# Optimization experiments

Hardware: AMD Instinct MI355X
Metric: run time of the kernel (lower is better)

Reference implementation:

```python
import jax, jax.numpy as jnp
import numpy as np

D = 128       # embed_dim
UD = 128      # user_embed_dim
NU, NI, NR = 100000, 50000, 10
B, H, S = 4096, 50, 32
EPS = 1e-5


def setup_inputs() -> dict:
    key = jax.random.key(0)
    ks = jax.random.split(key, 24)
    p = lambda k, s: (jax.random.normal(k, s, jnp.float32) * 0.05)
    inp = {
        'u2e': p(ks[0], (NU, D)), 'v2e': p(ks[1], (NI, D)), 'r2e': p(ks[2], (NR, D)),
        'gv_w1': p(ks[3], (2 * D, D)), 'gv_b1': jnp.zeros(D),
        'gv_w2': p(ks[4], (D, D)), 'gv_b2': jnp.zeros(D),
        'atth_w1': p(ks[5], (2 * D, D)), 'atth_b1': jnp.zeros(D),
        'atth_w2': p(ks[6], (D, 1)), 'atth_b2': jnp.zeros(1),
        'enc_w': p(ks[7], (2 * D, D)), 'enc_b': jnp.zeros(D),
        'atts_w1': p(ks[8], (2 * D, D)), 'atts_b1': jnp.zeros(D),
        'atts_w2': p(ks[9], (D, 1)), 'atts_b2': jnp.zeros(1),
        'soc_w': p(ks[10], (2 * D, D)), 'soc_b': jnp.zeros(D),
        'attn_wa': p(ks[11], (D, D)), 'attn_ba': p(ks[12], (D,)),
        'fc1_w': p(ks[13], (D, D)), 'fc1_b': jnp.zeros(D),
        'bn1_g': jnp.ones(D), 'bn1_b': jnp.zeros(D),
        'fc2_w': p(ks[14], (D, UD)), 'fc2_b': jnp.zeros(UD),
        'efc1_w': p(ks[15], (2 * UD, D)), 'efc1_b': jnp.zeros(D),
        'bn2_g': jnp.ones(D), 'bn2_b': jnp.zeros(D),
        'efc2_w': p(ks[16], (D, UD)), 'efc2_b': jnp.zeros(UD),
        'user_ids': jax.random.randint(ks[17], (B, 2), 0, NU),
        'hist_items': jax.random.randint(ks[18], (2 * B, H), 0, NI),
        'hist_ratings': jax.random.randint(ks[19], (2 * B, H), 0, NR),
        'soc_neigh': jax.random.randint(ks[20], (2 * B, S), 0, NU),
    }
    return inp


def _forward(u2e, v2e, r2e, gv_w1, gv_b1, gv_w2, gv_b2, atth_w1, atth_b1, atth_w2, atth_b2,
             enc_w, enc_b, atts_w1, atts_b1, atts_w2, atts_b2, soc_w, soc_b, attn_wa, attn_ba,
             fc1_w, fc1_b, bn1_g, bn1_b, fc2_w, fc2_b, efc1_w, efc1_b, bn2_g, bn2_b,
             efc2_w, efc2_b, user_ids, hist_items, hist_ratings, soc_neigh):
    u = u2e[user_ids.reshape(-1)]                                   # [N,D]
    # --- UV_Aggregator: rating-history aggregation with attention ---
    x = jnp.concatenate([v2e[hist_items], r2e[hist_ratings]], -1)   # [N,H,2D]
    x = jax.nn.relu(x @ gv_w1 + gv_b1)
    x = jax.nn.relu(x @ gv_w2 + gv_b2)                              # [N,H,D]
    q = jnp.broadcast_to(u[:, None, :], x.shape)
    e = jax.nn.relu(jnp.concatenate([x, q], -1) @ atth_w1 + atth_b1) @ atth_w2 + atth_b2
    a = jax.nn.softmax(e, axis=1)                                   # [N,H,1]
    agg = jnp.sum(a * x, axis=1)                                    # [N,D]
    # --- UV_Encoder ---
    h_hist = jax.nn.relu(jnp.concatenate([u, agg], -1) @ enc_w + enc_b)
    # --- Social_Aggregator: neighbor aggregation with attention ---
    nf = u2e[soc_neigh]                                             # [N,S,D]
    qn = jnp.broadcast_to(u[:, None, :], nf.shape)
    es = jax.nn.relu(jnp.concatenate([nf, qn], -1) @ atts_w1 + atts_b1) @ atts_w2 + atts_b2
    a_s = jax.nn.softmax(es, axis=1)
    agg_s = jnp.sum(a_s * nf, axis=1)                               # [N,D]
    # --- Social_Encoder ---
    h = jax.nn.relu(jnp.concatenate([h_hist, agg_s], -1) @ soc_w + soc_b)
    hp = h.reshape(-1, 2, D)                                        # [B,2,D] (initiator, respondent)
    # --- SelfAttentionBatch over each pair ---
    ap = jax.nn.softmax(jnp.tanh(hp @ attn_wa) @ attn_ba, axis=1)   # [B,2]
    w = ap[..., None] * hp                                          # [B,2,D]
    # --- social project head: fc1 -> BN (per-pair batch of 2, train mode) -> relu -> fc2 ---
    y = w @ fc1_w + fc1_b                                           # [B,2,D]
    mu = y.mean(axis=1, keepdims=True)
    var = y.var(axis=1, keepdims=True)
    y = (y - mu) * jax.lax.rsqrt(var + EPS) * bn1_g + bn1_b
    y = jax.nn.relu(y) @ fc2_w + fc2_b                              # [B,2,UD]
    ini, res = y[:, 0], y[:, 1]
    # --- esocial head on concatenated pair reps: fc -> BN over batch -> relu -> fc ---
    c = y.reshape(y.shape[0], -1)                                   # [B,2*UD]
    z = c @ efc1_w + efc1_b                                         # [B,D]
    z = (z - z.mean(0)) * jax.lax.rsqrt(z.var(0) + EPS) * bn2_g + bn2_b
    z = jax.nn.relu(z) @ efc2_w + efc2_b                            # [B,UD]
    return z, ini, res


def reference(u2e, v2e, r2e, gv_w1, gv_b1, gv_w2, gv_b2, atth_w1, atth_b1, atth_w2, atth_b2,
              enc_w, enc_b, atts_w1, atts_b1, atts_w2, atts_b2, soc_w, soc_b, attn_wa, attn_ba,
              fc1_w, fc1_b, bn1_g, bn1_b, fc2_w, fc2_b, efc1_w, efc1_b, bn2_g, bn2_b,
              efc2_w, efc2_b, user_ids, hist_items, hist_ratings, soc_neigh):
    return _forward(u2e, v2e, r2e, gv_w1, gv_b1, gv_w2, gv_b2, atth_w1, atth_b1, atth_w2,
                    atth_b2, enc_w, enc_b, atts_w1, atts_b1, atts_w2, atts_b2, soc_w, soc_b,
                    attn_wa, attn_ba, fc1_w, fc1_b, bn1_g, bn1_b, fc2_w, fc2_b, efc1_w,
                    efc1_b, bn2_g, bn2_b, efc2_w, efc2_b, user_ids, hist_items,
                    hist_ratings, soc_neigh)
```

## Files before the change

### kernel.cpp

```cpp
#include <hip/hip_runtime.h>
#include <hip/hip_bf16.h>
#include <math.h>

#define NROWS   8192
#define HLEN    50
#define SLEN    32
#define NPAIR   4096

typedef __attribute__((ext_vector_type(8))) short   short8;
typedef __attribute__((ext_vector_type(8))) __bf16  b8;
typedef __attribute__((ext_vector_type(4))) float   f32x4;
typedef unsigned short us;

#define A_GV_B1    0
#define A_GV_B2    128
#define A_ATTH_B1  256
#define A_ATTH_W2  384
#define A_ENC_W    512
#define A_ENC_B    33280
#define A_ATTS_B1  33408
#define A_ATTS_W2  33536
#define A_SOC_W    33664
#define A_SOC_B    66432
#define A_ATTN_WA  66560
#define A_ATTN_BA  82944
#define A_FC1_W    83072
#define A_FC1_B    99456
#define A_BN1_G    99584
#define A_BN1_B    99712
#define A_FC2_W    99840
#define A_FC2_B    116224
#define A_EFC1_W   116352
#define A_EFC1_B   149120
#define A_BN2_G    149248
#define A_BN2_B    149376
#define A_EFC2_W   149504
#define A_EFC2_B   165888
#define A_TOTAL    166016

#define WS_HR    0u
#define WS_Z     2097152u
#define WS_ST    4194304u
#define WS_WP1   4195328u
#define WS_WP2   4260864u
#define WS_WPA   4293632u
#define WS_WPS   4359168u
#define WS_AR    4424704u
#define WS_UB    4757504u
#define WS_VB    30357504u
#define WS_RB    43157504u
#define WS2_NEED 43160064u

__device__ __forceinline__ float b2f(us u){
  unsigned int x = ((unsigned int)u) << 16; float f;
  __builtin_memcpy(&f, &x, 4); return f;
}
__device__ __forceinline__ us f2b(float f){
  unsigned int x; __builtin_memcpy(&x, &f, 4);
  return (us)((x + 0x7fffu + ((x >> 16) & 1u)) >> 16);
}
__device__ __forceinline__ us f2bc(float f){
  unsigned int x; __builtin_memcpy(&x, &f, 4);
  return (us)((x + 0x8000u) >> 16);
}
__device__ __forceinline__ float relu(float x){ return 0.5f * (x + fabsf(x)); }

__device__ __forceinline__ b8 f8_to_b8(const float* f){
  short8 v;
#pragma unroll
  for (int j = 0; j < 8; ++j) v[j] = (short)f2bc(f[j]);
  return __builtin_bit_cast(b8, v);
}

typedef __attribute__((address_space(3))) unsigned char lds_b;
typedef const __attribute__((address_space(1))) unsigned char glob_b;

__device__ __forceinline__ void gll16(const us* g, us* d){
  __builtin_amdgcn_global_load_lds((glob_b*)g, (lds_b*)d, 16, 0, 0);
}

__device__ __forceinline__ void stage8k(const us* __restrict__ W, us* sB,
                                        int w, int l, int ks, int p){
  const us* src = W + ((long)ks << 12) + (w << 10) + (l << 3);
  us* dst = sB + (p << 12) + (w << 10);
  gll16(src,       dst);
  gll16(src + 512, dst + 512);
}

struct Tbl { const void* p[24]; unsigned off[25]; };
__global__ void k_cvt(Tbl tb, us* __restrict__ AR){
  int i = blockIdx.x * 256 + threadIdx.x;
  if (i >= A_TOTAL) return;
  int s = 0;
  while (i >= (int)tb.off[s + 1]) ++s;
  AR[i] = f2b(((const float*)tb.p[s])[i - (int)tb.off[s]]);
}

__global__ void k_pack(const float* __restrict__ W, us* __restrict__ Wp, int ksegs){
  int g = blockIdx.x * 256 + threadIdx.x;
  if (g >= ksegs * 512) return;
  int lane16 = g & 15, quad = (g >> 4) & 3, nt = (g >> 6) & 7, kseg = g >> 9;
#pragma unroll
  for (int j = 0; j < 8; ++j)
    Wp[(long)g * 8 + j] = f2b(W[(kseg * 32 + quad * 8 + j) * 128 + nt * 16 + lane16]);
}

__global__ void k_tab(const float* __restrict__ src, us* __restrict__ dst, int n8){
  int i = blockIdx.x * 256 + threadIdx.x;
  if (i >= n8) return;
  const float* s = src + (long)i * 8;
  short8 v;
#pragma unroll
  for (int j = 0; j < 8; ++j) v[j] = (short)f2b(s[j]);
  *(short8*)(dst + (long)i * 8) = v;
}

template<int TAB>
__global__ __launch_bounds__(256)
void k_fused(const int* __restrict__ items, const int* __restrict__ ratings,
             const void* __restrict__ vt, const void* __restrict__ rt,
             const int* __restrict__ uids, const void* __restrict__ ut,
             const int* __restrict__ soc,
             const us* __restrict__ Wp1, const us* __restrict__ Wp2,
             const us* __restrict__ WpA, const us* __restrict__ WpS,
             const us* __restrict__ AR, us* __restrict__ HR)
{
  const int r = blockIdx.x, t = threadIdx.x;
  const int w = t >> 6, l = t & 63, lane16 = l & 15, quad = l >> 4;
  const int tc = t & 127, th = t >> 7;
  const long ubase = (long)uids[r] * 128;

  __shared__ __align__(16) us sX[64 * 136];
  __shared__ __align__(16) us sB[2 * 4096];
  __shared__ float esh[64], a_sh[64], part[256], xin[256];

  const int arow = w * 16 + lane16;
  const bool av = arow < HLEN;
  const int it_i = av ? items[r * HLEN + arow]   : 0;
  const int rt_i = av ? ratings[r * HLEN + arow] : 0;

  b8 af[8];
#pragma unroll
  for (int ks = 0; ks < 8; ++ks){
    b8 a;
    if constexpr (TAB){
      const us* ap = (ks < 4)
          ? (const us*)vt + (long)it_i * 128 + ks * 32 + quad * 8
          : (const us*)rt + (long)rt_i * 128 + (ks - 4) * 32 + quad * 8;
      a = *(const b8*)ap;
    } else {
      const float* ap = (ks < 4)
          ? (const float*)vt + (long)it_i * 128 + ks * 32 + quad * 8
          : (const float*)rt + (long)rt_i * 128 + (ks - 4) * 32 + quad * 8;
      a = f8_to_b8(ap);
    }
    if (!av) a = __builtin_bit_cast(b8, (short8)0);
    af[ks] = a;
  }
  b8 uf[4];
#pragma unroll
  for (int ks = 0; ks < 4; ++ks){
    if constexpr (TAB)
      uf[ks] = *(const b8*)((const us*)ut + ubase + ks * 32 + quad * 8);
    else
      uf[ks] = f8_to_b8((const float*)ut + ubase + ks * 32 + quad * 8);
  }

  {
    f32x4 acc[8];
#pragma unroll
    for (int nt = 0; nt < 8; ++nt) acc[nt] = (f32x4){0.f,0.f,0.f,0.f};
    stage8k(Wp1, sB, w, l, 0, 0);
#pragma unroll
    for (int ks = 0; ks < 8; ++ks){
      __syncthreads();
      if (ks < 7) stage8k(Wp1, sB, w, l, ks + 1, (ks + 1) & 1);
      const us* bb = sB + ((ks & 1) << 12) + l * 8;
#pragma unroll
      for (int nt = 0; nt < 8; ++nt)
        acc[nt] = __builtin_amdgcn_mfma_f32_16x16x32_bf16(
            af[ks], *(const b8*)(bb + nt * 512), acc[nt], 0, 0, 0);
    }
#pragma unroll
    for (int nt = 0; nt < 8; ++nt){
      int col = nt * 16 + lane16;
      float bbv = b2f(AR[A_GV_B1 + col]);
#pragma unroll
      for (int rg = 0; rg < 4; ++rg)
        sX[(w * 16 + quad * 4 + rg) * 136 + col] = f2bc(relu(acc[nt][rg] + bbv));
    }
  }

  {
    b8 a2[4];
#pragma unroll
    for (int ks = 0; ks < 4; ++ks)
      a2[ks] = *(const b8*)(sX + arow * 136 + ks * 32 + quad * 8);
    f32x4 acc[8];
#pragma unroll
    for (int nt = 0; nt < 8; ++nt) acc[nt] = (f32x4){0.f,0.f,0.f,0.f};
    stage8k(Wp2, sB, w, l, 0, 0);
#pragma unroll
    for (int ks = 0; ks < 4; ++ks){
      __syncthreads();
      if (ks < 3) stage8k(Wp2, sB, w, l, ks + 1, (ks + 1) & 1);
      const us* bb = sB + ((ks & 1) << 12) + l * 8;
#pragma unroll
      for (int nt = 0; nt < 8; ++nt)
        acc[nt] = __builtin_amdgcn_mfma_f32_16x16x32_bf16(
            a2[ks], *(const b8*)(bb + nt * 512), acc[nt], 0, 0, 0);
    }
#pragma unroll
    for (int nt = 0; nt < 8; ++nt){
      int col = nt * 16 + lane16;
      float bbv = b2f(AR[A_GV_B2 + col]);
#pragma unroll
      for (int rg = 0; rg < 4; ++rg)
        sX[(w * 16 + quad * 4 + rg) * 136 + col] = f2bc(relu(acc[nt][rg] + bbv));
    }
  }

  {
    b8 a3[8];
#pragma unroll
    for (int ks = 0; ks < 4; ++ks)
      a3[ks] = *(const b8*)(sX + arow * 136 + ks * 32 + quad * 8);
#pragma unroll
    for (int ks = 0; ks < 4; ++ks) a3[4 + ks] = uf[ks];
    f32x4 acc[8];
#pragma unroll
    for (int nt = 0; nt < 8; ++nt) acc[nt] = (f32x4){0.f,0.f,0.f,0.f};
    stage8k(WpA, sB, w, l, 0, 0);
#pragma unroll
    for (int ks = 0; ks < 8; ++ks){
      __syncthreads();
      if (ks < 7) stage8k(WpA, sB, w, l, ks + 1, (ks + 1) & 1);
      const us* bb = sB + ((ks & 1) << 12) + l * 8;
#pragma unroll
      for (int nt = 0; nt < 8; ++nt)
        acc[nt] = __builtin_amdgcn_mfma_f32_16x16x32_bf16(
            a3[ks], *(const b8*)(bb + nt * 512), acc[nt], 0, 0, 0);
    }
    float pr[4] = {0.f, 0.f, 0.f, 0.f};
#pragma unroll
    for (int nt = 0; nt < 8; ++nt){
      int col = nt * 16 + lane16;
      float bbv = b2f(AR[A_ATTH_B1 + col]);
      float wwv = b2f(AR[A_ATTH_W2 + col]);
#pragma unroll
      for (int rg = 0; rg < 4; ++rg)
        pr[rg] += relu(acc[nt][rg] + bbv) * wwv;
    }
#pragma unroll
    for (int rg = 0; rg < 4; ++rg){
      float p = pr[rg];
      p += __shfl_xor(p, 1, 64);
      p += __shfl_xor(p, 2, 64);
      p += __shfl_xor(p, 4, 64);
      p += __shfl_xor(p, 8, 64);
      if (lane16 == 0) esh[w * 16 + quad * 4 + rg] = p;
    }
  }
  __syncthreads();

  if (t < 64){
    float e = (t < HLEN) ? esh[t] : -1e30f;
    float mx = e;
#pragma unroll
    for (int m = 1; m < 64; m <<= 1) mx = fmaxf(mx, __shfl_xor(mx, m, 64));
    float ex = (t < HLEN) ? expf(e - mx) : 0.f;
    float s = ex;
#pragma unroll
    for (int m = 1; m < 64; m <<= 1) s += __shfl_xor(s, m, 64);
    if (t < HLEN) a_sh[t] = ex / s;
  }
  __syncthreads();

  {
    float s = 0.f;
    for (int h = th * 25; h < th * 25 + 25; ++h)
      s += a_sh[h] * b2f(sX[h * 136 + tc]);
    part[t] = s;
  }
  __syncthreads();
  if (t < 128){
    xin[t] = TAB ? b2f(((const us*)ut)[ubase + t]) : ((const float*)ut)[ubase + t];
    xin[128 + t] = part[t] + part[128 + t];
  }
  __syncthreads();

  {
    float s0 = 0.f, s1 = 0.f;
    const int kb = th * 128;
    for (int k = 0; k < 128; k += 2){
      s0 += xin[kb + k]     * b2f(AR[A_ENC_W + (kb + k)     * 128 + tc]);
      s1 += xin[kb + k + 1] * b2f(AR[A_ENC_W + (kb + k + 1) * 128 + tc]);
    }
    part[t] = s0 + s1;
#pragma unroll
    for (int it = 0; it < 2; ++it){
      int idx = t * 8 + it * 2048;
      int row = idx >> 7, col = idx & 127;
      long eb = (long)soc[r * SLEN + row] * 128 + col;
      short8 v;
      if constexpr (TAB) v = *(const short8*)((const us*)ut + eb);
      else               v = __builtin_bit_cast(short8, f8_to_b8((const float*)ut + eb));
      *(short8*)(sX + row * 136 + col) = v;
    }
  }
  stage8k(WpS, sB, w, l, 0, 0);
  __syncthreads();

  float hhv = 0.f;
  if (t < 128)
    hhv = relu(part[t] + part[128 + t] + b2f(AR[A_ENC_B + t]));

  {
    const int mt = w & 1, nh = w >> 1;
    const int arow2 = mt * 16 + lane16;
    b8 aS[8];
#pragma unroll
    for (int ks = 0; ks < 4; ++ks)
      aS[ks] = *(const b8*)(sX + arow2 * 136 + ks * 32 + quad * 8);
#pragma unroll
    for (int ks = 0; ks < 4; ++ks) aS[4 + ks] = uf[ks];
    f32x4 acc[4];
#pragma unroll
    for (int nt = 0; nt < 4; ++nt) acc[nt] = (f32x4){0.f,0.f,0.f,0.f};
#pragma unroll
    for (int ks = 0; ks < 8; ++ks){
      __syncthreads();
      if (ks < 7) stage8k(WpS, sB, w, l, ks + 1, (ks + 1) & 1);
      const us* bb = sB + ((ks & 1) << 12) + (nh << 11) + l * 8;
#pragma unroll
      for (int nt = 0; nt < 4; ++nt)
        acc[nt] = __builtin_amdgcn_mfma_f32_16x16x32_bf16(
            aS[ks], *(const b8*)(bb + nt * 512), acc[nt], 0, 0, 0);
    }
    float pr[4] = {0.f, 0.f, 0.f, 0.f};
#pragma unroll
    for (int nt = 0; nt < 4; ++nt){
      int n = nh * 64 + nt * 16 + lane16;
      float bbv = b2f(AR[A_ATTS_B1 + n]);
      float wwv = b2f(AR[A_ATTS_W2 + n]);
#pragma unroll
      for (int rg = 0; rg < 4; ++rg)
        pr[rg] += relu(acc[nt][rg] + bbv) * wwv;
    }
#pragma unroll
    for (int rg = 0; rg < 4; ++rg){
      float p = pr[rg];
      p += __shfl_xor(p, 1, 64);
      p += __shfl_xor(p, 2, 64);
      p += __shfl_xor(p, 4, 64);
      p += __shfl_xor(p, 8, 64);
      if (lane16 == 0) esh[nh * 32 + mt * 16 + quad * 4 + rg] = p;
    }
  }
  __syncthreads();

  if (t < 32){
    float e = esh[t] + esh[32 + t];
    float mx = e;
#pragma unroll
    for (int m = 1; m < 32; m <<= 1) mx = fmaxf(mx, __shfl_xor(mx, m, 32));
    float ex = expf(e - mx);
    float s = ex;
#pragma unroll
    for (int m = 1; m < 32; m <<= 1) s += __shfl_xor(s, m, 32);
    a_sh[t] = ex / s;
  }
  __syncthreads();

  {
    float s = 0.f;
    for (int h = th * 16; h < th * 16 + 16; ++h)
      s += a_sh[h] * b2f(sX[h * 136 + tc]);
    part[t] = s;
  }
  __syncthreads();
  if (t < 128){
    xin[t]       = hhv;
    xin[128 + t] = part[t] + part[128 + t];
  }
  __syncthreads();

  {
    float s0 = 0.f, s1 = 0.f;
    const int kb = th * 128;
    for (int k = 0; k < 128; k += 2){
      s0 += xin[kb + k]     * b2f(AR[A_SOC_W + (kb + k)     * 128 + tc]);
      s1 += xin[kb + k + 1] * b2f(AR[A_SOC_W + (kb + k + 1) * 128 + tc]);
    }
    part[t] = s0 + s1;
  }
  __syncthreads();
  if (t < 128)
    HR[(long)r * 128 + t] =
        f2bc(relu(part[t] + part[128 + t] + b2f(AR[A_SOC_B + t])));
}

__global__ void k7_head(const us* __restrict__ HR, const us* __restrict__ AR,
                        float* __restrict__ OUT, float* __restrict__ Z)
{
  const int i = blockIdx.x, t = threadIdx.x;
  const int j = t >> 7, d = t & 127;
  __shared__ float hp[2][128], ysh[2][128], ry[2][128], csh[256], p2[2][128];
  __shared__ float sred[4];

  hp[j][d] = b2f(HR[(long)(2 * i + j) * 128 + d]);
  __syncthreads();

  float v0 = 0.f, v1 = 0.f;
  for (int k = 0; k < 128; k += 2){
    v0 += hp[j][k]     * b2f(AR[A_ATTN_WA + k * 128 + d]);
    v1 += hp[j][k + 1] * b2f(AR[A_ATTN_WA + (k + 1) * 128 + d]);
  }
  float part = tanhf(v0 + v1) * b2f(AR[A_ATTN_BA + d]);
#pragma unroll
  for (int m = 1; m < 64; m <<= 1) part += __shfl_xor(part, m, 64);
  if ((t & 63) == 0) sred[t >> 6] = part;
  __syncthreads();

  float s0 = sred[0] + sred[1], s1 = sred[2] + sred[3];
  float mx = fmaxf(s0, s1);
  float e0 = expf(s0 - mx), e1 = expf(s1 - mx);
  float aj = (j ? e1 : e0) / (e0 + e1);

  v0 = 0.f; v1 = 0.f;
  for (int k = 0; k < 128; k += 2){
    v0 += hp[j][k]     * b2f(AR[A_FC1_W + k * 128 + d]);
    v1 += hp[j][k + 1] * b2f(AR[A_FC1_W + (k + 1) * 128 + d]);
  }
  ysh[j][d] = aj * (v0 + v1) + b2f(AR[A_FC1_B + d]);
  __syncthreads();

  if (t < 128){
    float y0 = ysh[0][t], y1 = ysh[1][t];
    float mu = 0.5f * (y0 + y1);
    float dv = 0.5f * (y0 - y1);
    float rs = rsqrtf(dv * dv + 1e-5f);
    float g = b2f(AR[A_BN1_G + t]), bb = b2f(AR[A_BN1_B + t]);
    ry[0][t] = relu((y0 - mu) * rs * g + bb);
    ry[1][t] = relu((y1 - mu) * rs * g + bb);
  }
  __syncthreads();

  v0 = 0.f; v1 = 0.f;
  for (int k = 0; k < 128; k += 2){
    v0 += ry[j][k]     * b2f(AR[A_FC2_W + k * 128 + d]);
    v1 += ry[j][k + 1] * b2f(AR[A_FC2_W + (k + 1) * 128 + d]);
  }
  float y2 = v0 + v1 + b2f(AR[A_FC2_B + d]);
  OUT[(long)(j ? 2 * NPAIR * 128 : NPAIR * 128) + (long)i * 128 + d] = y2;
  csh[j * 128 + d] = y2;
  __syncthreads();

  {
    const int kh = t >> 7, d2 = t & 127;
    v0 = 0.f; v1 = 0.f;
    for (int k = 0; k < 128; k += 2){
      v0 += csh[kh * 128 + k]     * b2f(AR[A_EFC1_W + (kh * 128 + k) * 128 + d2]);
      v1 += csh[kh * 128 + k + 1] * b2f(AR[A_EFC1_W + (kh * 128 + k + 1) * 128 + d2]);
    }
    p2[kh][d2] = v0 + v1;
  }
  __syncthreads();
  if (t < 128)
    Z[(long)i * 128 + t] = p2[0][t] + p2[1][t] + b2f(AR[A_EFC1_B + t]);
}

__global__ void k8_stats(const float* __restrict__ Z, float* __restrict__ ST){
  const int c = blockIdx.x, t = threadIdx.x;
  float s = 0.f, s2 = 0.f;
  for (int row = t; row < NPAIR; row += 256){
    float v = Z[(long)row * 128 + c];
    s += v; s2 += v * v;
  }
#pragma unroll
  for (int m = 1; m < 64; m <<= 1){ s += __shfl_xor(s, m, 64); s2 += __shfl_xor(s2, m, 64); }
  __shared__ float red[8];
  if ((t & 63) == 0){ red[t >> 6] = s; red[4 + (t >> 6)] = s2; }
  __syncthreads();
  if (t == 0){
    float S  = red[0] + red[1] + red[2] + red[3];
    float S2 = red[4] + red[5] + red[6] + red[7];
    float mean = S / (float)NPAIR;
    float var  = S2 / (float)NPAIR - mean * mean;
    ST[c]       = mean;
    ST[128 + c] = rsqrtf(var + 1e-5f);
  }
}

__global__ void k9_final(const float* __restrict__ Z, const float* __restrict__ ST,
                         const us* __restrict__ AR, float* __restrict__ OUT)
{
  const int i = blockIdx.x, t = threadIdx.x;
  __shared__ float zn[128];
  float zv = Z[(long)i * 128 + t];
  zn[t] = relu((zv - ST[t]) * ST[128 + t] * b2f(AR[A_BN2_G + t]) + b2f(AR[A_BN2_B + t]));
  __syncthreads();
  float v0 = 0.f, v1 = 0.f;
  for (int k = 0; k < 128; k += 2){
    v0 += zn[k]     * b2f(AR[A_EFC2_W + k * 128 + t]);
    v1 += zn[k + 1] * b2f(AR[A_EFC2_W + (k + 1) * 128 + t]);
  }
  OUT[(long)i * 128 + t] = v0 + v1 + b2f(AR[A_EFC2_B + t]);
}

extern "C" void kernel_launch(void* const* d_in, const int* in_sizes, int n_in,
                              void* d_out, int out_size, void* d_ws, size_t ws_size,
                              hipStream_t stream)
{
  const float* u2e = (const float*)d_in[0];
  const float* v2e = (const float*)d_in[1];
  const float* r2e = (const float*)d_in[2];
  const int* user_ids     = (const int*)d_in[33];
  const int* hist_items   = (const int*)d_in[34];
  const int* hist_ratings = (const int*)d_in[35];
  const int* soc_neigh    = (const int*)d_in[36];

  char* ws = (char*)d_ws;
  us*    HR  = (us*)(ws + WS_HR);
  float* Z   = (float*)(ws + WS_Z);
  float* ST  = (float*)(ws + WS_ST);
  us*    Wp1 = (us*)(ws + WS_WP1);
  us*    Wp2 = (us*)(ws + WS_WP2);
  us*    WpA = (us*)(ws + WS_WPA);
  us*    WpS = (us*)(ws + WS_WPS);
  us*    AR  = (us*)(ws + WS_AR);
  us*    Ub  = (us*)(ws + WS_UB);
  us*    Vb  = (us*)(ws + WS_VB);
  us*    Rb  = (us*)(ws + WS_RB);
  float* OUT = (float*)d_out;

  const bool big = ws_size >= (size_t)WS2_NEED;

  Tbl tb;
  const void* sp[24] = {d_in[4], d_in[6], d_in[8], d_in[9], d_in[11], d_in[12],
                        d_in[14], d_in[15], d_in[17], d_in[18], d_in[19], d_in[20],
                        d_in[21], d_in[22], d_in[23], d_in[24], d_in[25], d_in[26],
                        d_in[27], d_in[28], d_in[29], d_in[30], d_in[31], d_in[32]};
  const unsigned offs[25] = {0,128,256,384,512,33280,33408,33536,33664,66432,
                             66560,82944,83072,99456,99584,99712,99840,116224,
                             116352,149120,149248,149376,149504,165888,166016};
  for (int i = 0; i < 24; ++i) tb.p[i] = sp[i];
  for (int i = 0; i < 25; ++i) tb.off[i] = offs[i];
  k_cvt<<<(A_TOTAL + 255) / 256, 256, 0, stream>>>(tb, AR);

  k_pack<<<16, 256, 0, stream>>>((const float*)d_in[3],  Wp1, 8);
  k_pack<<< 8, 256, 0, stream>>>((const float*)d_in[5],  Wp2, 4);
  k_pack<<<16, 256, 0, stream>>>((const float*)d_in[7],  WpA, 8);
  k_pack<<<16, 256, 0, stream>>>((const float*)d_in[13], WpS, 8);

  if (big){
    k_tab<<<(1600000 + 255) / 256, 256, 0, stream>>>(u2e, Ub, 1600000);
    k_tab<<<( 800000 + 255) / 256, 256, 0, stream>>>(v2e, Vb,  800000);
    k_tab<<<(    160 + 255) / 256, 256, 0, stream>>>(r2e, Rb,     160);
    k_fused<1><<<NROWS, 256, 0, stream>>>(hist_items, hist_ratings, Vb, Rb,
        user_ids, Ub, soc_neigh, Wp1, Wp2, WpA, WpS, AR, HR);
  } else {
    k_fused<0><<<NROWS, 256, 0, stream>>>(hist_items, hist_ratings, v2e, r2e,
        user_ids, u2e, soc_neigh, Wp1, Wp2, WpA, WpS, AR, HR);
  }

  k7_head<<<NPAIR, 256, 0, stream>>>(HR, AR, OUT, Z);
  k8_stats<<<128, 256, 0, stream>>>(Z, ST);
  k9_final<<<NPAIR, 128, 0, stream>>>(Z, ST, AR, OUT);
}
```

Measured before the change: 552.1 us.

## Process two rows per 512-thread block sharing staged weight tiles

The fused kernel now runs 512 threads per block and handles two user rows, one per half-block. Each weight k-slice is staged into shared memory once and used by both rows, so each thread issues one global-to-LDS load instead of two. This halves weight staging traffic and block count. In exchange it doubles per-block LDS for the activation buffers and makes every barrier span 8 waves, which may reduce occupancy or add sync stalls.

```diff
diff --git a/kernel.cpp b/kernel.cpp
--- a/kernel.cpp
+++ b/kernel.cpp
@@ -80,11 +80,10 @@
 }
 
 __device__ __forceinline__ void stage8k(const us* __restrict__ W, us* sB,
-                                        int w, int l, int ks, int p){
-  const us* src = W + ((long)ks << 12) + (w << 10) + (l << 3);
-  us* dst = sB + (p << 12) + (w << 10);
-  gll16(src,       dst);
-  gll16(src + 512, dst + 512);
+                                        int w8, int l, int ks, int p){
+  const us* src = W + ((long)ks << 12) + (w8 << 9) + (l << 3);
+  us* dst = sB + (p << 12) + (w8 << 9);
+  gll16(src, dst);
 }
 
 struct Tbl { const void* p[24]; unsigned off[25]; };
@@ -116,7 +115,7 @@
 }
 
 template<int TAB>
-__global__ __launch_bounds__(256)
+__global__ __launch_bounds__(512)
 void k_fused(const int* __restrict__ items, const int* __restrict__ ratings,
              const void* __restrict__ vt, const void* __restrict__ rt,
              const int* __restrict__ uids, const void* __restrict__ ut,
@@ -125,14 +124,18 @@
              const us* __restrict__ WpA, const us* __restrict__ WpS,
              const us* __restrict__ AR, us* __restrict__ HR)
 {
-  const int r = blockIdx.x, t = threadIdx.x;
-  const int w = t >> 6, l = t & 63, lane16 = l & 15, quad = l >> 4;
-  const int tc = t & 127, th = t >> 7;
+  const int t = threadIdx.x;
+  const int rr = t >> 8, tt = t & 255;
+  const int r = blockIdx.x * 2 + rr;
+  const int w = tt >> 6;
+  const int w8 = t >> 6;
+  const int l = t & 63, lane16 = l & 15, quad = l >> 4;
+  const int tc = tt & 127, th = tt >> 7;
   const long ubase = (long)uids[r] * 128;
 
-  __shared__ __align__(16) us sX[64 * 136];
+  __shared__ __align__(16) us sX[2][64 * 136];
   __shared__ __align__(16) us sB[2 * 4096];
-  __shared__ float esh[64], a_sh[64], part[256], xin[256];
+  __shared__ float esh[2][64], a_sh[2][64], part[2][256], xin[2][256];
 
   const int arow = w * 16 + lane16;
   const bool av = arow < HLEN;
@@ -170,11 +173,11 @@
     f32x4 acc[8];
 #pragma unroll
     for (int nt = 0; nt < 8; ++nt) acc[nt] = (f32x4){0.f,0.f,0.f,0.f};
-    stage8k(Wp1, sB, w, l, 0, 0);
+    stage8k(Wp1, sB, w8, l, 0, 0);
 #pragma unroll
     for (int ks = 0; ks < 8; ++ks){
       __syncthreads();
-      if (ks < 7) stage8k(Wp1, sB, w, l, ks + 1, (ks + 1) & 1);
+      if (ks < 7) stage8k(Wp1, sB, w8, l, ks + 1, (ks + 1) & 1);
       const us* bb = sB + ((ks & 1) << 12) + l * 8;
 #pragma unroll
       for (int nt = 0; nt < 8; ++nt)
@@ -187,7 +190,7 @@
       float bbv = b2f(AR[A_GV_B1 + col]);
 #pragma unroll
       for (int rg = 0; rg < 4; ++rg)
-        sX[(w * 16 + quad * 4 + rg) * 136 + col] = f2bc(relu(acc[nt][rg] + bbv));
+        sX[rr][(w * 16 + quad * 4 + rg) * 136 + col] = f2bc(relu(acc[nt][rg] + bbv));
     }
   }
 
@@ -195,15 +198,15 @@
     b8 a2[4];
 #pragma unroll
     for (int ks = 0; ks < 4; ++ks)
-      a2[ks] = *(const b8*)(sX + arow * 136 + ks * 32 + quad * 8);
+      a2[ks] = *(const b8*)(sX[rr] + arow * 136 + ks * 32 + quad * 8);
     f32x4 acc[8];
 #pragma unroll
     for (int nt = 0; nt < 8; ++nt) acc[nt] = (f32x4){0.f,0.f,0.f,0.f};
-    stage8k(Wp2, sB, w, l, 0, 0);
+    stage8k(Wp2, sB, w8, l, 0, 0);
 #pragma unroll
     for (int ks = 0; ks < 4; ++ks){
       __syncthreads();
-      if (ks < 3) stage8k(Wp2, sB, w, l, ks + 1, (ks + 1) & 1);
+      if (ks < 3) stage8k(Wp2, sB, w8, l, ks + 1, (ks + 1) & 1);
       const us* bb = sB + ((ks & 1) << 12) + l * 8;
 #pragma unroll
       for (int nt = 0; nt < 8; ++nt)
@@ -216,7 +219,7 @@
       float bbv = b2f(AR[A_GV_B2 + col]);
 #pragma unroll
       for (int rg = 0; rg < 4; ++rg)
-        sX[(w * 16 + quad * 4 + rg) * 136 + col] = f2bc(relu(acc[nt][rg] + bbv));
+        sX[rr][(w * 16 + quad * 4 + rg) * 136 + col] = f2bc(relu(acc[nt][rg] + bbv));
     }
   }
 
@@ -224,17 +227,17 @@
     b8 a3[8];
 #pragma unroll
     for (int ks = 0; ks < 4; ++ks)
-      a3[ks] = *(const b8*)(sX + arow * 136 + ks * 32 + quad * 8);
+      a3[ks] = *(const b8*)(sX[rr] + arow * 136 + ks * 32 + quad * 8);
 #pragma unroll
     for (int ks = 0; ks < 4; ++ks) a3[4 + ks] = uf[ks];
     f32x4 acc[8];
 #pragma unroll
     for (int nt = 0; nt < 8; ++nt) acc[nt] = (f32x4){0.f,0.f,0.f,0.f};
-    stage8k(WpA, sB, w, l, 0, 0);
+    stage8k(WpA, sB, w8, l, 0, 0);
 #pragma unroll
     for (int ks = 0; ks < 8; ++ks){
       __syncthreads();
-      if (ks < 7) stage8k(WpA, sB, w, l, ks + 1, (ks + 1) & 1);
+      if (ks < 7) stage8k(WpA, sB, w8, l, ks + 1, (ks + 1) & 1);
       const us* bb = sB + ((ks & 1) << 12) + l * 8;
 #pragma unroll
       for (int nt = 0; nt < 8; ++nt)
@@ -258,34 +261,34 @@
       p += __shfl_xor(p, 2, 64);
       p += __shfl_xor(p, 4, 64);
       p += __shfl_xor(p, 8, 64);
-      if (lane16 == 0) esh[w * 16 + quad * 4 + rg] = p;
-    }
-  }
-  __syncthreads();
-
-  if (t < 64){
-    float e = (t < HLEN) ? esh[t] : -1e30f;
+      if (lane16 == 0) esh[rr][w * 16 + quad * 4 + rg] = p;
+    }
+  }
+  __syncthreads();
+
+  if (tt < 64){
+    float e = (tt < HLEN) ? esh[rr][tt] : -1e30f;
     float mx = e;
 #pragma unroll
     for (int m = 1; m < 64; m <<= 1) mx = fmaxf(mx, __shfl_xor(mx, m, 64));
-    float ex = (t < HLEN) ? expf(e - mx) : 0.f;
+    float ex = (tt < HLEN) ? expf(e - mx) : 0.f;
     float s = ex;
 #pragma unroll
     for (int m = 1; m < 64; m <<= 1) s += __shfl_xor(s, m, 64);
-    if (t < HLEN) a_sh[t] = ex / s;
+    if (tt < HLEN) a_sh[rr][tt] = ex / s;
   }
   __syncthreads();
 
   {
     float s = 0.f;
     for (int h = th * 25; h < th * 25 + 25; ++h)
-      s += a_sh[h] * b2f(sX[h * 136 + tc]);
-    part[t] = s;
-  }
-  __syncthreads();
-  if (t < 128){
-    xin[t] = TAB ? b2f(((const us*)ut)[ubase + t]) : ((const float*)ut)[ubase + t];
-    xin[128 + t] = part[t] + part[128 + t];
+      s += a_sh[rr][h] * b2f(sX[rr][h * 136 + tc]);
+    part[rr][tt] = s;
+  }
+  __syncthreads();
+  if (tt < 128){
+    xin[rr][tt] = TAB ? b2f(((const us*)ut)[ubase + tt]) : ((const float*)ut)[ubase + tt];
+    xin[rr][128 + tt] = part[rr][tt] + part[rr][128 + tt];
   }
   __syncthreads();
 
@@ -293,27 +296,27 @@
     float s0 = 0.f, s1 = 0.f;
     const int kb = th * 128;
     for (int k = 0; k < 128; k += 2){
-      s0 += xin[kb + k]     * b2f(AR[A_ENC_W + (kb + k)     * 128 + tc]);
-      s1 += xin[kb + k + 1] * b2f(AR[A_ENC_W + (kb + k + 1) * 128 + tc]);
-    }
-    part[t] = s0 + s1;
+      s0 += xin[rr][kb + k]     * b2f(AR[A_ENC_W + (kb + k)     * 128 + tc]);
+      s1 += xin[rr][kb + k + 1] * b2f(AR[A_ENC_W + (kb + k + 1) * 128 + tc]);
+    }
+    part[rr][tt] = s0 + s1;
 #pragma unroll
     for (int it = 0; it < 2; ++it){
-      int idx = t * 8 + it * 2048;
+      int idx = tt * 8 + it * 2048;
       int row = idx >> 7, col = idx & 127;
       long eb = (long)soc[r * SLEN + row] * 128 + col;
       short8 v;
       if constexpr (TAB) v = *(const short8*)((const us*)ut + eb);
       else               v = __builtin_bit_cast(short8, f8_to_b8((const float*)ut + eb));
-      *(short8*)(sX + row * 136 + col) = v;
-    }
-  }
-  stage8k(WpS, sB, w, l, 0, 0);
+      *(short8*)(sX[rr] + row * 136 + col) = v;
+    }
+  }
+  stage8k(WpS, sB, w8, l, 0, 0);
   __syncthreads();
 
   float hhv = 0.f;
-  if (t < 128)
-    hhv = relu(part[t] + part[128 + t] + b2f(AR[A_ENC_B + t]));
+  if (tt < 128)
+    hhv = relu(part[rr][tt] + part[rr][128 + tt] + b2f(AR[A_ENC_B + tt]));
 
   {
     const int mt = w & 1, nh = w >> 1;
@@ -321,7 +324,7 @@
     b8 aS[8];
 #pragma unroll
     for (int ks = 0; ks < 4; ++ks)
-      aS[ks] = *(const b8*)(sX + arow2 * 136 + ks * 32 + quad * 8);
+      aS[ks] = *(const b8*)(sX[rr] + arow2 * 136 + ks * 32 + quad * 8);
 #pragma unroll
     for (int ks = 0; ks < 4; ++ks) aS[4 + ks] = uf[ks];
     f32x4 acc[4];
@@ -330,7 +333,7 @@
 #pragma unroll
     for (int ks = 0; ks < 8; ++ks){
       __syncthreads();
-      if (ks < 7) stage8k(WpS, sB, w, l, ks + 1, (ks + 1) & 1);
+      if (ks < 7) stage8k(WpS, sB, w8, l, ks + 1, (ks + 1) & 1);
       const us* bb = sB + ((ks & 1) << 12) + (nh << 11) + l * 8;
 #pragma unroll
       for (int nt = 0; nt < 4; ++nt)
@@ -354,13 +357,13 @@
       p += __shfl_xor(p, 2, 64);
       p += __shfl_xor(p, 4, 64);
       p += __shfl_xor(p, 8, 64);
-      if (lane16 == 0) esh[nh * 32 + mt * 16 + quad * 4 + rg] = p;
-    }
-  }
-  __syncthreads();
-
-  if (t < 32){
-    float e = esh[t] + esh[32 + t];
+      if (lane16 == 0) esh[rr][nh * 32 + mt * 16 + quad * 4 + rg] = p;
+    }
+  }
+  __syncthreads();
+
+  if (tt < 32){
+    float e = esh[rr][tt] + esh[rr][32 + tt];
     float mx = e;
 #pragma unroll
     for (int m = 1; m < 32; m <<= 1) mx = fmaxf(mx, __shfl_xor(mx, m, 32));
@@ -368,20 +371,20 @@
     float s = ex;
 #pragma unroll
     for (int m = 1; m < 32; m <<= 1) s += __shfl_xor(s, m, 32);
-    a_sh[t] = ex / s;
+    a_sh[rr][tt] = ex / s;
   }
   __syncthreads();
 
   {
     float s = 0.f;
     for (int h = th * 16; h < th * 16 + 16; ++h)
-      s += a_sh[h] * b2f(sX[h * 136 + tc]);
-    part[t] = s;
-  }
-  __syncthreads();
-  if (t < 128){
-    xin[t]       = hhv;
-    xin[128 + t] = part[t] + part[128 + t];
+      s += a_sh[rr][h] * b2f(sX[rr][h * 136 + tc]);
+    part[rr][tt] = s;
+  }
+  __syncthreads();
+  if (tt < 128){
+    xin[rr][tt]       = hhv;
+    xin[rr][128 + tt] = part[rr][tt] + part[rr][128 + tt];
   }
   __syncthreads();
 
@@ -389,15 +392,15 @@
     float s0 = 0.f, s1 = 0.f;
     const int kb = th * 128;
     for (int k = 0; k < 128; k += 2){
-      s0 += xin[kb + k]     * b2f(AR[A_SOC_W + (kb + k)     * 128 + tc]);
-      s1 += xin[kb + k + 1] * b2f(AR[A_SOC_W + (kb + k + 1) * 128 + tc]);
-    }
-    part[t] = s0 + s1;
-  }
-  __syncthreads();
-  if (t < 128)
-    HR[(long)r * 128 + t] =
-        f2bc(relu(part[t] + part[128 + t] + b2f(AR[A_SOC_B + t])));
+      s0 += xin[rr][kb + k]     * b2f(AR[A_SOC_W + (kb + k)     * 128 + tc]);
+      s1 += xin[rr][kb + k + 1] * b2f(AR[A_SOC_W + (kb + k + 1) * 128 + tc]);
+    }
+    part[rr][tt] = s0 + s1;
+  }
+  __syncthreads();
+  if (tt < 128)
+    HR[(long)r * 128 + tt] =
+        f2bc(relu(part[rr][tt] + part[rr][128 + tt] + b2f(AR[A_SOC_B + tt])));
 }
 
 __global__ void k7_head(const us* __restrict__ HR, const us* __restrict__ AR,
@@ -557,10 +560,10 @@
     k_tab<<<(1600000 + 255) / 256, 256, 0, stream>>>(u2e, Ub, 1600000);
     k_tab<<<( 800000 + 255) / 256, 256, 0, stream>>>(v2e, Vb,  800000);
     k_tab<<<(    160 + 255) / 256, 256, 0, stream>>>(r2e, Rb,     160);
-    k_fused<1><<<NROWS, 256, 0, stream>>>(hist_items, hist_ratings, Vb, Rb,
+    k_fused<1><<<NROWS / 2, 512, 0, stream>>>(hist_items, hist_ratings, Vb, Rb,
         user_ids, Ub, soc_neigh, Wp1, Wp2, WpA, WpS, AR, HR);
   } else {
-    k_fused<0><<<NROWS, 256, 0, stream>>>(hist_items, hist_ratings, v2e, r2e,
+    k_fused<0><<<NROWS / 2, 512, 0, stream>>>(hist_items, hist_ratings, v2e, r2e,
         user_ids, u2e, soc_neigh, Wp1, Wp2, WpA, WpS, AR, HR);
   }
 
```

Result: faster. 499.3 us (-9.6%).
